# Kernel optimization log

Measured on AMD Instinct MI355X. Metric: run time of the kernel, lower is better.

Reference implementation:

```python
import jax, jax.numpy as jnp
import numpy as np

EMBED = 1024
HEADS = 16
HEAD_DIM = EMBED // HEADS


def setup_inputs() -> dict:
    key = jax.random.key(0)
    ks = jax.random.split(key, 5)
    s = 1.0 / np.sqrt(EMBED)
    return {
        "x": jax.random.normal(ks[0], (4, 2048, EMBED), dtype=jnp.float32),
        "W_qkv": jax.random.uniform(ks[1], (EMBED, 3 * EMBED), jnp.float32, -s, s),
        "b_qkv": jax.random.uniform(ks[2], (3 * EMBED,), jnp.float32, -s, s),
        "W_out": jax.random.uniform(ks[3], (EMBED, EMBED), jnp.float32, -s, s),
        "b_out": jax.random.uniform(ks[4], (EMBED,), jnp.float32, -s, s),
    }


def reference(x, W_qkv, b_qkv, W_out, b_out):
    B, S, E = x.shape
    qkv = x @ W_qkv + b_qkv  # [B,S,3E]
    q, k, v = jnp.split(qkv, 3, axis=-1)
    # [B,S,E] -> [B,H,S,D]
    def split_heads(t):
        return t.reshape(B, S, HEADS, HEAD_DIM).transpose(0, 2, 1, 3)
    q, k, v = split_heads(q), split_heads(k), split_heads(v)
    scale = 1.0 / jnp.sqrt(jnp.asarray(HEAD_DIM, dtype=x.dtype))
    scores = jnp.einsum("bhqd,bhkd->bhqk", q, k) * scale
    attn = jax.nn.softmax(scores, axis=-1)
    out = jnp.einsum("bhqk,bhkd->bhqd", attn, v)
    out = out.transpose(0, 2, 1, 3).reshape(B, S, E)
    return out @ W_out + b_out
```

## Files before the change

### kernel.cpp

```cpp
#include <hip/hip_runtime.h>
#include <hip/hip_bf16.h>

typedef __bf16 bf16;
typedef __bf16 bf16x8 __attribute__((ext_vector_type(8)));
typedef float f32x4 __attribute__((ext_vector_type(4)));
typedef float f32x16 __attribute__((ext_vector_type(16)));

#define EMB 1024
#define SEQ 2048
#define NH 16
#define HD 64
#define MTOK 8192

__global__ __launch_bounds__(256) void prep(const float* __restrict__ x, bf16* __restrict__ xb,
                                            const float* __restrict__ Wq, bf16* __restrict__ WqT,
                                            const float* __restrict__ Wo, bf16* __restrict__ WoT) {
    __shared__ float tile[32][33];
    int bid = blockIdx.x;
    if (bid < 4096) {
        int i = bid * 256 + threadIdx.x;
        const float4* p = (const float4*)x + 2 * (size_t)i;
        float4 a = p[0], b = p[1];
        bf16x8 v;
        v[0] = (bf16)a.x; v[1] = (bf16)a.y; v[2] = (bf16)a.z; v[3] = (bf16)a.w;
        v[4] = (bf16)b.x; v[5] = (bf16)b.y; v[6] = (bf16)b.z; v[7] = (bf16)b.w;
        *(bf16x8*)(xb + 8 * (size_t)i) = v;
        return;
    }
    const float* W;
    bf16* Wt;
    int K = EMB, N, n0, k0;
    if (bid < 4096 + 3072) {
        int i = bid - 4096;
        W = Wq; Wt = WqT; N = 3 * EMB;
        n0 = (i % 96) * 32; k0 = (i / 96) * 32;
    } else {
        int i = bid - 7168;
        W = Wo; Wt = WoT; N = EMB;
        n0 = (i & 31) * 32; k0 = (i >> 5) * 32;
    }
    int tx = threadIdx.x & 31, ty = threadIdx.x >> 5;
    #pragma unroll
    for (int i = 0; i < 32; i += 8)
        tile[ty + i][tx] = W[(size_t)(k0 + ty + i) * N + n0 + tx];
    __syncthreads();
    #pragma unroll
    for (int i = 0; i < 32; i += 8)
        Wt[(size_t)(n0 + ty + i) * K + k0 + tx] = (bf16)tile[tx][ty + i];
}

#define BM 128
#define BN 128
#define BK 64
#define LDK 72

#define QSCALE 0.1803368801111f

__global__ __launch_bounds__(256) void gemm_qkv(const bf16* __restrict__ A,
                                                const bf16* __restrict__ Bt,
                                                const float* __restrict__ bias,
                                                bf16* __restrict__ qws, bf16* __restrict__ kws,
                                                bf16* __restrict__ vt) {
    __shared__ bf16 sA[BM][LDK];
    __shared__ bf16 sB[BN][LDK];
    const int K = 1024;
    int lin = blockIdx.x + 64 * blockIdx.y;
    int a8 = lin & 7, tt = lin >> 3;
    int mx = (a8 << 3) + (tt & 7), ny = tt >> 3;
    int m0 = mx * BM, n0 = ny * BN;
    int t = threadIdx.x, lane = t & 63, w = t >> 6;
    int wr = w >> 1, wc = w & 1;
    int l15 = lane & 15, quad = lane >> 4;

    f32x4 acc[4][4];
    #pragma unroll
    for (int i = 0; i < 4; i++)
        #pragma unroll
        for (int j = 0; j < 4; j++) acc[i][j] = (f32x4){0.f, 0.f, 0.f, 0.f};

    int srow = t >> 3, sc8 = (t & 7) * 8;
    for (int kt = 0; kt < K; kt += BK) {
        #pragma unroll
        for (int p = 0; p < 4; p++) {
            int r = srow + p * 32;
            *(uint4*)&sA[r][sc8] = *(const uint4*)(A + (size_t)(m0 + r) * K + kt + sc8);
            *(uint4*)&sB[r][sc8] = *(const uint4*)(Bt + (size_t)(n0 + r) * K + kt + sc8);
        }
        __syncthreads();
        #pragma unroll
        for (int ks = 0; ks < BK; ks += 32) {
            int kk = ks + quad * 8;
            bf16x8 af[4], bfr[4];
            #pragma unroll
            for (int mt = 0; mt < 4; mt++) af[mt] = *(const bf16x8*)&sA[wr * 64 + mt * 16 + l15][kk];
            #pragma unroll
            for (int nt = 0; nt < 4; nt++) bfr[nt] = *(const bf16x8*)&sB[wc * 64 + nt * 16 + l15][kk];
            #pragma unroll
            for (int mt = 0; mt < 4; mt++)
                #pragma unroll
                for (int nt = 0; nt < 4; nt++)
                    acc[mt][nt] = __builtin_amdgcn_mfma_f32_16x16x32_bf16(af[mt], bfr[nt], acc[mt][nt], 0, 0, 0);
        }
        __syncthreads();
    }
    #pragma unroll
    for (int mt = 0; mt < 4; mt++)
        #pragma unroll
        for (int nt = 0; nt < 4; nt++) {
            int col = n0 + wc * 64 + nt * 16 + l15;
            float bv = bias[col];
            int mat = col >> 10;
            int e = col & 1023;
            int h = e >> 6, d = e & 63;
            int row0 = m0 + wr * 64 + mt * 16 + quad * 4;
            int bb = row0 >> 11, s0 = row0 & 2047;
            int bh = bb * NH + h;
            float vv[4];
            #pragma unroll
            for (int r = 0; r < 4; r++) vv[r] = acc[mt][nt][r] + bv;
            if (mat == 0) {
                #pragma unroll
                for (int r = 0; r < 4; r++)
                    qws[((size_t)bh * SEQ + s0 + r) * HD + d] = (bf16)(vv[r] * QSCALE);
            } else if (mat == 1) {
                #pragma unroll
                for (int r = 0; r < 4; r++)
                    kws[((size_t)bh * SEQ + s0 + r) * HD + d] = (bf16)vv[r];
            } else {
                ushort4 pk;
                pk.x = __builtin_bit_cast(unsigned short, (bf16)vv[0]);
                pk.y = __builtin_bit_cast(unsigned short, (bf16)vv[1]);
                pk.z = __builtin_bit_cast(unsigned short, (bf16)vv[2]);
                pk.w = __builtin_bit_cast(unsigned short, (bf16)vv[3]);
                *(ushort4*)((unsigned short*)vt + ((size_t)bh * HD + d) * SEQ + s0) = pk;
            }
        }
}

__device__ __forceinline__ unsigned pk2(float a, float b) {
    unsigned lo = (unsigned)__builtin_bit_cast(unsigned short, (bf16)a);
    unsigned hi = (unsigned)__builtin_bit_cast(unsigned short, (bf16)b);
    return lo | (hi << 16);
}

__global__ __launch_bounds__(256, 4) void attn(const bf16* __restrict__ qws, const bf16* __restrict__ kws,
                                               const bf16* __restrict__ vt, bf16* __restrict__ ao) {
    __shared__ bf16 sK[2][64][72];
    __shared__ bf16 sVt[2][64][72];

    int lin = blockIdx.x + (SEQ / 128) * blockIdx.y;
    int a8 = lin & 7, tt = lin >> 3;
    int bh = (a8 << 3) + (tt >> 4);
    int q0 = (tt & 15) * 128;
    int t = threadIdx.x, lane = t & 63, w = t >> 6;
    int l31 = lane & 31, hi = lane >> 5;

    const bf16* qb = qws + (size_t)bh * SEQ * HD;
    const bf16* kb = kws + (size_t)bh * SEQ * HD;
    const bf16* vtb = vt + (size_t)bh * HD * SEQ;

    bf16x8 qf[4];
    #pragma unroll
    for (int ks = 0; ks < 4; ks++)
        qf[ks] = *(const bf16x8*)(qb + (size_t)(q0 + w * 32 + l31) * HD + ks * 16 + hi * 8);

    f32x16 o[2];
    float lsum = 0.f;
    #pragma unroll
    for (int mt = 0; mt < 2; mt++)
        #pragma unroll
        for (int r = 0; r < 16; r++) o[mt][r] = 0.f;

    int krow = t >> 3, kc8 = (t & 7) * 8;
    int vdr = t >> 2, vc16 = (t & 3) * 16;

    {
        uint4 k0 = *(const uint4*)(kb + (size_t)krow * HD + kc8);
        uint4 k1 = *(const uint4*)(kb + (size_t)(krow + 32) * HD + kc8);
        const bf16* src = vtb + (size_t)vdr * SEQ + vc16;
        uint4 v0 = *(const uint4*)src;
        uint4 v1 = *(const uint4*)(src + 8);
        *(uint4*)&sK[0][krow][kc8] = k0;
        *(uint4*)&sK[0][krow + 32][kc8] = k1;
        *(uint4*)&sVt[0][vdr][vc16] = v0;
        *(uint4*)&sVt[0][vdr][vc16 + 8] = v1;
    }

    int cur = 0;
    for (int kv0 = 0; kv0 < SEQ; kv0 += 64) {
        __syncthreads();

        int nxt = kv0 + 64;
        uint4 nk0, nk1, nv0, nv1;
        if (nxt < SEQ) {
            nk0 = *(const uint4*)(kb + (size_t)(nxt + krow) * HD + kc8);
            nk1 = *(const uint4*)(kb + (size_t)(nxt + krow + 32) * HD + kc8);
            const bf16* src = vtb + (size_t)vdr * SEQ + nxt + vc16;
            nv0 = *(const uint4*)src;
            nv1 = *(const uint4*)(src + 8);
        }

        f32x16 sacc[2];
        #pragma unroll
        for (int nt = 0; nt < 2; nt++)
            #pragma unroll
            for (int r = 0; r < 16; r++) sacc[nt][r] = 0.f;
        __builtin_amdgcn_s_setprio(1);
        #pragma unroll
        for (int ks = 0; ks < 4; ks++)
            #pragma unroll
            for (int nt = 0; nt < 2; nt++) {
                bf16x8 kf = *(const bf16x8*)&sK[cur][nt * 32 + l31][ks * 16 + hi * 8];
                sacc[nt] = __builtin_amdgcn_mfma_f32_32x32x16_bf16(kf, qf[ks], sacc[nt], 0, 0, 0);
            }
        __builtin_amdgcn_s_setprio(0);

        bf16x8 pb[4];
        #pragma unroll
        for (int nt = 0; nt < 2; nt++) {
            float e[16];
            #pragma unroll
            for (int r = 0; r < 16; r++) {
                e[r] = __builtin_amdgcn_exp2f(sacc[nt][r]);
                lsum += e[r];
            }
            #pragma unroll
            for (int blk = 0; blk < 2; blk++) {
                int b = blk * 8;
                unsigned a0 = pk2(e[b + 0], e[b + 1]);
                unsigned a1 = pk2(e[b + 2], e[b + 3]);
                unsigned b0 = pk2(e[b + 4], e[b + 5]);
                unsigned b1 = pk2(e[b + 6], e[b + 7]);
                asm("v_permlane32_swap_b32 %0, %1" : "+v"(a0), "+v"(b0));
                asm("v_permlane32_swap_b32 %0, %1" : "+v"(a1), "+v"(b1));
                uint4 f;
                f.x = a0; f.y = a1; f.z = b0; f.w = b1;
                pb[nt * 2 + blk] = __builtin_bit_cast(bf16x8, f);
            }
        }

        __builtin_amdgcn_s_setprio(1);
        #pragma unroll
        for (int s = 0; s < 4; s++)
            #pragma unroll
            for (int mt = 0; mt < 2; mt++) {
                bf16x8 vf = *(const bf16x8*)&sVt[cur][mt * 32 + l31][s * 16 + hi * 8];
                o[mt] = __builtin_amdgcn_mfma_f32_32x32x16_bf16(vf, pb[s], o[mt], 0, 0, 0);
            }
        __builtin_amdgcn_s_setprio(0);

        if (nxt < SEQ) {
            *(uint4*)&sK[cur ^ 1][krow][kc8] = nk0;
            *(uint4*)&sK[cur ^ 1][krow + 32][kc8] = nk1;
            *(uint4*)&sVt[cur ^ 1][vdr][vc16] = nv0;
            *(uint4*)&sVt[cur ^ 1][vdr][vc16 + 8] = nv1;
        }
        cur ^= 1;
    }

    float inv = __builtin_amdgcn_rcpf(lsum + __shfl_xor(lsum, 32));

    int h = bh & 15, bb = bh >> 4;
    int q = q0 + w * 32 + l31;
    #pragma unroll
    for (int mt = 0; mt < 2; mt++)
        #pragma unroll
        for (int g = 0; g < 4; g++) {
            ushort4 pk;
            pk.x = __builtin_bit_cast(unsigned short, (bf16)(o[mt][4 * g + 0] * inv));
            pk.y = __builtin_bit_cast(unsigned short, (bf16)(o[mt][4 * g + 1] * inv));
            pk.z = __builtin_bit_cast(unsigned short, (bf16)(o[mt][4 * g + 2] * inv));
            pk.w = __builtin_bit_cast(unsigned short, (bf16)(o[mt][4 * g + 3] * inv));
            *(ushort4*)((unsigned short*)ao + ((size_t)(bb * SEQ + q)) * EMB + h * HD + mt * 32 + 8 * g + 4 * hi) = pk;
        }
}

__global__ __launch_bounds__(256) void gemm_out(const bf16* __restrict__ A,
                                                const bf16* __restrict__ Bt,
                                                const float* __restrict__ bias,
                                                float* __restrict__ out) {
    __shared__ bf16 sA[BM][LDK];
    __shared__ bf16 sB[BN][LDK];
    const int K = 1024;
    int lin = blockIdx.x + 64 * blockIdx.y;
    int a8 = lin & 7, tt = lin >> 3;
    int mx = (a8 << 3) + (tt & 7), ny = tt >> 3;
    int m0 = mx * BM, n0 = ny * BN;
    int t = threadIdx.x, lane = t & 63, w = t >> 6;
    int wr = w >> 1, wc = w & 1;
    int l15 = lane & 15, quad = lane >> 4;

    f32x4 acc[4][4];
    #pragma unroll
    for (int i = 0; i < 4; i++)
        #pragma unroll
        for (int j = 0; j < 4; j++) acc[i][j] = (f32x4){0.f, 0.f, 0.f, 0.f};

    int srow = t >> 3, sc8 = (t & 7) * 8;
    for (int kt = 0; kt < K; kt += BK) {
        #pragma unroll
        for (int p = 0; p < 4; p++) {
            int r = srow + p * 32;
            *(uint4*)&sA[r][sc8] = *(const uint4*)(A + (size_t)(m0 + r) * K + kt + sc8);
            *(uint4*)&sB[r][sc8] = *(const uint4*)(Bt + (size_t)(n0 + r) * K + kt + sc8);
        }
        __syncthreads();
        #pragma unroll
        for (int ks = 0; ks < BK; ks += 32) {
            int kk = ks + quad * 8;
            bf16x8 af[4], bfr[4];
            #pragma unroll
            for (int mt = 0; mt < 4; mt++) af[mt] = *(const bf16x8*)&sA[wr * 64 + mt * 16 + l15][kk];
            #pragma unroll
            for (int nt = 0; nt < 4; nt++) bfr[nt] = *(const bf16x8*)&sB[wc * 64 + nt * 16 + l15][kk];
            #pragma unroll
            for (int mt = 0; mt < 4; mt++)
                #pragma unroll
                for (int nt = 0; nt < 4; nt++)
                    acc[mt][nt] = __builtin_amdgcn_mfma_f32_16x16x32_bf16(af[mt], bfr[nt], acc[mt][nt], 0, 0, 0);
        }
        __syncthreads();
    }
    #pragma unroll
    for (int mt = 0; mt < 4; mt++)
        #pragma unroll
        for (int nt = 0; nt < 4; nt++) {
            int col = n0 + wc * 64 + nt * 16 + l15;
            float bv = bias[col];
            #pragma unroll
            for (int r = 0; r < 4; r++) {
                int row = m0 + wr * 64 + mt * 16 + quad * 4 + r;
                out[(size_t)row * EMB + col] = acc[mt][nt][r] + bv;
            }
        }
}

extern "C" void kernel_launch(void* const* d_in, const int* in_sizes, int n_in,
                              void* d_out, int out_size, void* d_ws, size_t ws_size,
                              hipStream_t stream) {
    const float* x     = (const float*)d_in[0];
    const float* W_qkv = (const float*)d_in[1];
    const float* b_qkv = (const float*)d_in[2];
    const float* W_out = (const float*)d_in[3];
    const float* b_out = (const float*)d_in[4];
    float* out = (float*)d_out;

    char* ws = (char*)d_ws;
    bf16* xb    = (bf16*)(ws);
    bf16* wqkvT = (bf16*)(ws + (size_t)(16 << 20));
    bf16* woutT = (bf16*)(ws + (size_t)(22 << 20));
    bf16* qws   = (bf16*)(ws + (size_t)(24 << 20));
    bf16* kws   = (bf16*)(ws + (size_t)(40 << 20));
    bf16* vt    = (bf16*)(ws + (size_t)(56 << 20));
    bf16* aow   = (bf16*)(ws + (size_t)(72 << 20));

    prep<<<8192, 256, 0, stream>>>(x, xb, W_qkv, wqkvT, W_out, woutT);
    gemm_qkv<<<dim3(MTOK / BM, 3 * EMB / BN), 256, 0, stream>>>(xb, wqkvT, b_qkv, qws, kws, vt);
    attn<<<dim3(SEQ / 128, 64), 256, 0, stream>>>(qws, kws, vt, aow);
    gemm_out<<<dim3(MTOK / BM, EMB / BN), 256, 0, stream>>>(aow, woutT, b_out, out);
}
```

Measured before the change: 267.5 us.

## Drop LDS staging in attention; read K/V fragments directly from global

The attention kernel no longer stages K and V^T tiles through double-buffered shared memory with block barriers. Each wave now loads its MFMA operand fragments straight from global memory, relying on L1/L2 for reuse. Blocks shrink to 128 threads (two waves, 64 queries), which doubles the grid to keep occupancy up. This removes LDS traffic and __syncthreads, but each wave now re-fetches K/V from cache with strided, less coalesced loads, and there is no software prefetch to hide latency.

```diff
diff --git a/kernel.cpp b/kernel.cpp
--- a/kernel.cpp
+++ b/kernel.cpp
@@ -143,15 +143,12 @@
     return lo | (hi << 16);
 }
 
-__global__ __launch_bounds__(256, 4) void attn(const bf16* __restrict__ qws, const bf16* __restrict__ kws,
+__global__ __launch_bounds__(128, 4) void attn(const bf16* __restrict__ qws, const bf16* __restrict__ kws,
                                                const bf16* __restrict__ vt, bf16* __restrict__ ao) {
-    __shared__ bf16 sK[2][64][72];
-    __shared__ bf16 sVt[2][64][72];
-
-    int lin = blockIdx.x + (SEQ / 128) * blockIdx.y;
+    int lin = blockIdx.x + (SEQ / 64) * blockIdx.y;
     int a8 = lin & 7, tt = lin >> 3;
-    int bh = (a8 << 3) + (tt >> 4);
-    int q0 = (tt & 15) * 128;
+    int bh = (a8 << 3) + (tt >> 5);
+    int q0 = (tt & 31) * 64;
     int t = threadIdx.x, lane = t & 63, w = t >> 6;
     int l31 = lane & 31, hi = lane >> 5;
 
@@ -171,35 +168,7 @@
         #pragma unroll
         for (int r = 0; r < 16; r++) o[mt][r] = 0.f;
 
-    int krow = t >> 3, kc8 = (t & 7) * 8;
-    int vdr = t >> 2, vc16 = (t & 3) * 16;
-
-    {
-        uint4 k0 = *(const uint4*)(kb + (size_t)krow * HD + kc8);
-        uint4 k1 = *(const uint4*)(kb + (size_t)(krow + 32) * HD + kc8);
-        const bf16* src = vtb + (size_t)vdr * SEQ + vc16;
-        uint4 v0 = *(const uint4*)src;
-        uint4 v1 = *(const uint4*)(src + 8);
-        *(uint4*)&sK[0][krow][kc8] = k0;
-        *(uint4*)&sK[0][krow + 32][kc8] = k1;
-        *(uint4*)&sVt[0][vdr][vc16] = v0;
-        *(uint4*)&sVt[0][vdr][vc16 + 8] = v1;
-    }
-
-    int cur = 0;
     for (int kv0 = 0; kv0 < SEQ; kv0 += 64) {
-        __syncthreads();
-
-        int nxt = kv0 + 64;
-        uint4 nk0, nk1, nv0, nv1;
-        if (nxt < SEQ) {
-            nk0 = *(const uint4*)(kb + (size_t)(nxt + krow) * HD + kc8);
-            nk1 = *(const uint4*)(kb + (size_t)(nxt + krow + 32) * HD + kc8);
-            const bf16* src = vtb + (size_t)vdr * SEQ + nxt + vc16;
-            nv0 = *(const uint4*)src;
-            nv1 = *(const uint4*)(src + 8);
-        }
-
         f32x16 sacc[2];
         #pragma unroll
         for (int nt = 0; nt < 2; nt++)
@@ -210,7 +179,7 @@
         for (int ks = 0; ks < 4; ks++)
             #pragma unroll
             for (int nt = 0; nt < 2; nt++) {
-                bf16x8 kf = *(const bf16x8*)&sK[cur][nt * 32 + l31][ks * 16 + hi * 8];
+                bf16x8 kf = *(const bf16x8*)(kb + (size_t)(kv0 + nt * 32 + l31) * HD + ks * 16 + hi * 8);
                 sacc[nt] = __builtin_amdgcn_mfma_f32_32x32x16_bf16(kf, qf[ks], sacc[nt], 0, 0, 0);
             }
         __builtin_amdgcn_s_setprio(0);
@@ -244,18 +213,10 @@
         for (int s = 0; s < 4; s++)
             #pragma unroll
             for (int mt = 0; mt < 2; mt++) {
-                bf16x8 vf = *(const bf16x8*)&sVt[cur][mt * 32 + l31][s * 16 + hi * 8];
+                bf16x8 vf = *(const bf16x8*)(vtb + (size_t)(mt * 32 + l31) * SEQ + kv0 + s * 16 + hi * 8);
                 o[mt] = __builtin_amdgcn_mfma_f32_32x32x16_bf16(vf, pb[s], o[mt], 0, 0, 0);
             }
         __builtin_amdgcn_s_setprio(0);
-
-        if (nxt < SEQ) {
-            *(uint4*)&sK[cur ^ 1][krow][kc8] = nk0;
-            *(uint4*)&sK[cur ^ 1][krow + 32][kc8] = nk1;
-            *(uint4*)&sVt[cur ^ 1][vdr][vc16] = nv0;
-            *(uint4*)&sVt[cur ^ 1][vdr][vc16 + 8] = nv1;
-        }
-        cur ^= 1;
     }
 
     float inv = __builtin_amdgcn_rcpf(lsum + __shfl_xor(lsum, 32));
@@ -356,6 +317,6 @@
 
     prep<<<8192, 256, 0, stream>>>(x, xb, W_qkv, wqkvT, W_out, woutT);
     gemm_qkv<<<dim3(MTOK / BM, 3 * EMB / BN), 256, 0, stream>>>(xb, wqkvT, b_qkv, qws, kws, vt);
-    attn<<<dim3(SEQ / 128, 64), 256, 0, stream>>>(qws, kws, vt, aow);
+    attn<<<dim3(SEQ / 64, 64), 128, 0, stream>>>(qws, kws, vt, aow);
     gemm_out<<<dim3(MTOK / BM, EMB / BN), 256, 0, stream>>>(aow, woutT, b_out, out);
 }
```

New measurement: 420.9 us. 57.3% more time.

## Double-buffer GEMM tiles with direct global-to-LDS loads and MFMA priority

Applied to the files above, without the earlier changes.

Both projection GEMMs now stage A and B tiles straight from global memory into LDS with global_load_lds and use two LDS buffers, so the next K-tile is fetched while MFMAs run on the current one. This removes the register round-trip and the separate load-then-barrier stage in each iteration. The row padding is dropped because the direct-to-LDS path needs contiguous rows, which may bring LDS bank conflicts on the fragment reads. s_setprio raises wave priority during the MFMA section.

```diff
diff --git a/kernel.cpp b/kernel.cpp
--- a/kernel.cpp
+++ b/kernel.cpp
@@ -11,6 +11,11 @@
 #define NH 16
 #define HD 64
 #define MTOK 8192
+
+__device__ __forceinline__ void gload16(const bf16* g, bf16* l) {
+    __builtin_amdgcn_global_load_lds((const __attribute__((address_space(1))) unsigned int*)g,
+                                     (__attribute__((address_space(3))) unsigned int*)l, 16, 0, 0);
+}
 
 __global__ __launch_bounds__(256) void prep(const float* __restrict__ x, bf16* __restrict__ xb,
                                             const float* __restrict__ Wq, bf16* __restrict__ WqT,
@@ -52,7 +57,6 @@
 #define BM 128
 #define BN 128
 #define BK 64
-#define LDK 72
 
 #define QSCALE 0.1803368801111f
 
@@ -61,8 +65,8 @@
                                                 const float* __restrict__ bias,
                                                 bf16* __restrict__ qws, bf16* __restrict__ kws,
                                                 bf16* __restrict__ vt) {
-    __shared__ bf16 sA[BM][LDK];
-    __shared__ bf16 sB[BN][LDK];
+    __shared__ bf16 sA[2][BM][BK];
+    __shared__ bf16 sB[2][BN][BK];
     const int K = 1024;
     int lin = blockIdx.x + 64 * blockIdx.y;
     int a8 = lin & 7, tt = lin >> 3;
@@ -78,30 +82,44 @@
         #pragma unroll
         for (int j = 0; j < 4; j++) acc[i][j] = (f32x4){0.f, 0.f, 0.f, 0.f};
 
-    int srow = t >> 3, sc8 = (t & 7) * 8;
+    int crow = lane >> 3, ccol = (lane & 7) * 8;
+    const bf16* gA = A + (size_t)(m0 + w * 32 + crow) * K + ccol;
+    const bf16* gB = Bt + (size_t)(n0 + w * 32 + crow) * K + ccol;
+
+    #pragma unroll
+    for (int j = 0; j < 4; j++) {
+        gload16(gA + (size_t)(j * 8) * K, &sA[0][w * 32 + j * 8][0]);
+        gload16(gB + (size_t)(j * 8) * K, &sB[0][w * 32 + j * 8][0]);
+    }
+    __syncthreads();
+
+    int cur = 0;
     for (int kt = 0; kt < K; kt += BK) {
-        #pragma unroll
-        for (int p = 0; p < 4; p++) {
-            int r = srow + p * 32;
-            *(uint4*)&sA[r][sc8] = *(const uint4*)(A + (size_t)(m0 + r) * K + kt + sc8);
-            *(uint4*)&sB[r][sc8] = *(const uint4*)(Bt + (size_t)(n0 + r) * K + kt + sc8);
-        }
-        __syncthreads();
+        if (kt + BK < K) {
+            #pragma unroll
+            for (int j = 0; j < 4; j++) {
+                gload16(gA + (size_t)(j * 8) * K + kt + BK, &sA[cur ^ 1][w * 32 + j * 8][0]);
+                gload16(gB + (size_t)(j * 8) * K + kt + BK, &sB[cur ^ 1][w * 32 + j * 8][0]);
+            }
+        }
+        __builtin_amdgcn_s_setprio(1);
         #pragma unroll
         for (int ks = 0; ks < BK; ks += 32) {
             int kk = ks + quad * 8;
             bf16x8 af[4], bfr[4];
             #pragma unroll
-            for (int mt = 0; mt < 4; mt++) af[mt] = *(const bf16x8*)&sA[wr * 64 + mt * 16 + l15][kk];
-            #pragma unroll
-            for (int nt = 0; nt < 4; nt++) bfr[nt] = *(const bf16x8*)&sB[wc * 64 + nt * 16 + l15][kk];
+            for (int mt = 0; mt < 4; mt++) af[mt] = *(const bf16x8*)&sA[cur][wr * 64 + mt * 16 + l15][kk];
+            #pragma unroll
+            for (int nt = 0; nt < 4; nt++) bfr[nt] = *(const bf16x8*)&sB[cur][wc * 64 + nt * 16 + l15][kk];
             #pragma unroll
             for (int mt = 0; mt < 4; mt++)
                 #pragma unroll
                 for (int nt = 0; nt < 4; nt++)
                     acc[mt][nt] = __builtin_amdgcn_mfma_f32_16x16x32_bf16(af[mt], bfr[nt], acc[mt][nt], 0, 0, 0);
         }
+        __builtin_amdgcn_s_setprio(0);
         __syncthreads();
+        cur ^= 1;
     }
     #pragma unroll
     for (int mt = 0; mt < 4; mt++)
@@ -279,8 +297,8 @@
                                                 const bf16* __restrict__ Bt,
                                                 const float* __restrict__ bias,
                                                 float* __restrict__ out) {
-    __shared__ bf16 sA[BM][LDK];
-    __shared__ bf16 sB[BN][LDK];
+    __shared__ bf16 sA[2][BM][BK];
+    __shared__ bf16 sB[2][BN][BK];
     const int K = 1024;
     int lin = blockIdx.x + 64 * blockIdx.y;
     int a8 = lin & 7, tt = lin >> 3;
@@ -296,30 +314,44 @@
         #pragma unroll
         for (int j = 0; j < 4; j++) acc[i][j] = (f32x4){0.f, 0.f, 0.f, 0.f};
 
-    int srow = t >> 3, sc8 = (t & 7) * 8;
+    int crow = lane >> 3, ccol = (lane & 7) * 8;
+    const bf16* gA = A + (size_t)(m0 + w * 32 + crow) * K + ccol;
+    const bf16* gB = Bt + (size_t)(n0 + w * 32 + crow) * K + ccol;
+
+    #pragma unroll
+    for (int j = 0; j < 4; j++) {
+        gload16(gA + (size_t)(j * 8) * K, &sA[0][w * 32 + j * 8][0]);
+        gload16(gB + (size_t)(j * 8) * K, &sB[0][w * 32 + j * 8][0]);
+    }
+    __syncthreads();
+
+    int cur = 0;
     for (int kt = 0; kt < K; kt += BK) {
-        #pragma unroll
-        for (int p = 0; p < 4; p++) {
-            int r = srow + p * 32;
-            *(uint4*)&sA[r][sc8] = *(const uint4*)(A + (size_t)(m0 + r) * K + kt + sc8);
-            *(uint4*)&sB[r][sc8] = *(const uint4*)(Bt + (size_t)(n0 + r) * K + kt + sc8);
-        }
-        __syncthreads();
+        if (kt + BK < K) {
+            #pragma unroll
+            for (int j = 0; j < 4; j++) {
+                gload16(gA + (size_t)(j * 8) * K + kt + BK, &sA[cur ^ 1][w * 32 + j * 8][0]);
+                gload16(gB + (size_t)(j * 8) * K + kt + BK, &sB[cur ^ 1][w * 32 + j * 8][0]);
+            }
+        }
+        __builtin_amdgcn_s_setprio(1);
         #pragma unroll
         for (int ks = 0; ks < BK; ks += 32) {
             int kk = ks + quad * 8;
             bf16x8 af[4], bfr[4];
             #pragma unroll
-            for (int mt = 0; mt < 4; mt++) af[mt] = *(const bf16x8*)&sA[wr * 64 + mt * 16 + l15][kk];
-            #pragma unroll
-            for (int nt = 0; nt < 4; nt++) bfr[nt] = *(const bf16x8*)&sB[wc * 64 + nt * 16 + l15][kk];
+            for (int mt = 0; mt < 4; mt++) af[mt] = *(const bf16x8*)&sA[cur][wr * 64 + mt * 16 + l15][kk];
+            #pragma unroll
+            for (int nt = 0; nt < 4; nt++) bfr[nt] = *(const bf16x8*)&sB[cur][wc * 64 + nt * 16 + l15][kk];
             #pragma unroll
             for (int mt = 0; mt < 4; mt++)
                 #pragma unroll
                 for (int nt = 0; nt < 4; nt++)
                     acc[mt][nt] = __builtin_amdgcn_mfma_f32_16x16x32_bf16(af[mt], bfr[nt], acc[mt][nt], 0, 0, 0);
         }
+        __builtin_amdgcn_s_setprio(0);
         __syncthreads();
+        cur ^= 1;
     }
     #pragma unroll
     for (int mt = 0; mt < 4; mt++)
```

Result: slower. 285.3 us (+6.6%).
